# Kernel optimization log

Measured on AMD Instinct MI355X. Metric: run time of the kernel, lower is better.

Reference implementation:

```python
import jax, jax.numpy as jnp
import numpy as np

# WFN symmetry table: symmetry index -> (px, py, pz) angular-momentum exponents
# (s; px,py,pz; 6 cartesian d; 10 cartesian f) as in standard .wfn files.
WFN_SYMMETRY_INDEX = np.array([
    [0, 0, 0],
    [1, 0, 0], [0, 1, 0], [0, 0, 1],
    [2, 0, 0], [0, 2, 0], [0, 0, 2], [1, 1, 0], [1, 0, 1], [0, 1, 1],
    [3, 0, 0], [0, 3, 0], [0, 0, 3], [2, 1, 0], [2, 0, 1], [0, 2, 1],
    [1, 2, 0], [1, 0, 2], [0, 1, 2], [1, 1, 1],
], dtype=np.float32)


def setup_inputs() -> dict:
    key = jax.random.key(0)
    k1, k2, k3, k4, k5 = jax.random.split(key, 5)
    n, ms, na, nps = 16, 4096, 32, 512
    dv = jax.random.normal(k1, (n, ms, na, 3), jnp.float32)          # sample->atom displacement vectors
    centers = jax.random.randint(k2, (n, nps), 0, na)                # primitive -> atom index (-1 = pad)
    exp = jax.random.uniform(k3, (n, nps), jnp.float32)              # GTO exponents (>0)
    sym = jax.random.randint(k4, (n, nps), 0, 20)                    # symmetry index into WFN table
    dm = jax.random.normal(k5, (n, nps, nps), jnp.float32) / nps     # density matrices
    return {"dv": dv, "centers": centers, "exp": exp, "sym": sym, "dm": dm}


def _density(dv, exp, dm, centers, sym):
    # dv: [n,ms,na,3]; exp: [n,np]; dm: [n,np,np]; centers/sym: [n,np] int
    sym_map = jnp.asarray(WFN_SYMMETRY_INDEX)
    valid = centers >= 0                                   # padded primitives marked -1
    c = jnp.where(valid, centers, 0)
    s = jnp.where(valid, sym, 0)
    r2 = jnp.sum(dv * dv, axis=-1)                         # [n,ms,na] squared distances
    r2g = jax.vmap(lambda r, ci: r[:, ci])(r2, c)          # [n,ms,np] gather per primitive
    dvg = jax.vmap(lambda d, ci: d[:, ci])(dv, c)          # [n,ms,np,3]
    pw = sym_map[s]                                        # [n,np,3] angular exponents
    # GTO kernel: dx^px * dy^py * dz^pz * exp(-alpha * r^2)
    ang = jnp.prod(jnp.power(dvg, pw[:, None, :, :]), axis=-1)   # [n,ms,np]
    basis = ang * jnp.exp(-exp[:, None, :] * r2g)
    basis = basis * valid[:, None, :].astype(basis.dtype)        # zero out padded primitives
    # rho = sum_pq basis_p * dm_pq * basis_q (per molecule, per sample point)
    return jnp.einsum('nmp,npq,nmq->nm', basis, dm, basis)


def reference(dv, centers, exp, sym, dm):
    return _density(dv, exp, dm, centers, sym)
```

## Files before the change

kernel.cpp:

```cpp
#include <hip/hip_runtime.h>
#include <stdint.h>

#define NMOL 16
#define MS   4096
#define NA   32
#define NP   512
#define BM   64
#define TBL  65536u

typedef __attribute__((ext_vector_type(4))) float  f32x4;
typedef __attribute__((ext_vector_type(4))) unsigned int u32x4;
typedef __attribute__((ext_vector_type(2))) unsigned int u32x2;
typedef __attribute__((ext_vector_type(8))) short  s16x8;
typedef unsigned int uint;
typedef unsigned short ushort;

#define WS_DMF_OFF   0u
#define WS_DMF_SZ    (16u*512u*512u*2u)
#define WS_M2A_OFF   (WS_DMF_OFF + WS_DMF_SZ)
#define WS_M2A_SZ    (16u*512u*4u)
#define WS_M2B_OFF   (WS_M2A_OFF + WS_M2A_SZ)
#define WS_M2B_SZ    (16u*512u*4u)
#define WS_ALPH_OFF  (WS_M2B_OFF + WS_M2B_SZ)

__device__ __constant__ uint c_pw[20] = {
  0x000,
  0x001, 0x010, 0x100,
  0x002, 0x020, 0x200, 0x011, 0x101, 0x110,
  0x003, 0x030, 0x300, 0x012, 0x102, 0x120, 0x021, 0x201, 0x210, 0x111
};

__device__ __forceinline__ ushort f2bf(float f) {
  uint u = __float_as_uint(f);
  u = u + 0x7fffu + ((u >> 16) & 1u);
  return (ushort)(u >> 16);
}
__device__ __forceinline__ float bflo(uint u) { return __uint_as_float(u << 16); }
__device__ __forceinline__ float bfhi(uint u) { return __uint_as_float(u & 0xFFFF0000u); }
__device__ __forceinline__ float cvt16lo(uint u) {
  float r; asm("v_cvt_f32_f16 %0, %1" : "=v"(r) : "v"(u)); return r;
}
__device__ __forceinline__ float cvt16hi(uint u) {
  uint s = u >> 16; float r; asm("v_cvt_f32_f16 %0, %1" : "=v"(r) : "v"(s)); return r;
}
__device__ __forceinline__ uint pkmul(uint a, uint b) {
  uint r; asm("v_pk_mul_f16 %0, %1, %2" : "=v"(r) : "v"(a), "v"(b)); return r;
}
__device__ __forceinline__ s16x8 mkfrag(u32x2 lo, u32x2 hi) {
  union { uint u[4]; s16x8 v; } x;
  x.u[0] = lo[0]; x.u[1] = lo[1]; x.u[2] = hi[0]; x.u[3] = hi[1];
  return x.v;
}

__global__ void dm_pack(const float* __restrict__ dm, short* __restrict__ dmF) {
  __shared__ float tile[NP * 16];
  const int Q = blockIdx.x, n = blockIdx.y;
  const float* src = dm + (size_t)n * NP * NP + Q * 16;
#pragma unroll
  for (int i = 0; i < 32; ++i) {
    int e = threadIdx.x + 256 * i;
    int p = e >> 4, c = e & 15;
    tile[e] = src[(size_t)p * NP + c];
  }
  __syncthreads();
  short* dst = dmF + ((size_t)(n * 32 + Q) * 16) * 512;
#pragma unroll
  for (int i = 0; i < 4; ++i) {
    int v = threadIdx.x + 256 * i;
    int kblk = v >> 6, l = v & 63;
    int p0 = kblk * 32 + ((l >> 4) << 3);
    int col = l & 15;
    s16x8 o;
#pragma unroll
    for (int j = 0; j < 8; ++j) o[j] = (short)f2bf(tile[(p0 + j) * 16 + col]);
    *(s16x8*)(dst + (size_t)v * 8) = o;
  }
}

__global__ void prep_pack(const int* __restrict__ centers, const int* __restrict__ sym,
                          const float* __restrict__ expg,
                          uint* __restrict__ m2a, uint* __restrict__ m2b,
                          float* __restrict__ alphaS) {
  int i = blockIdx.x * 256 + threadIdx.x;
  int craw = centers[i], s = sym[i];
  bool valid = (craw >= 0);
  uint c = (uint)((valid ? craw : 0) & (NA - 1));
  int si = valid ? s : 0;
  si = (si >= 0 && si < 20) ? si : 0;
  uint pw = c_pw[si];
  uint px = pw & 15u, py = (pw >> 4) & 15u, pz = (pw >> 8) & 15u;
  uint d = px + py + pz;
  uint h[3]; int k = 0;
#pragma unroll
  for (uint ax = 0; ax < 3; ++ax) {
    uint e = (pw >> (4 * ax)) & 15u;
    for (uint r = 0; r < e; ++r) if (k < 3) h[k++] = c * 512u + ax * 128u;
  }
  while (k < 3) h[k++] = c * 512u;
  m2a[i] = h[0] | (h[1] << 16);
  m2b[i] = h[2] | (d << 14) | (c << 16);
  alphaS[i] = (valid ? -expg[i] : -1e5f) * 1.44269504088896f;
}

__launch_bounds__(512, 4)
__global__ void wfn_fused8(const float* __restrict__ dv,
                           const uint* __restrict__ m2aG,
                           const uint* __restrict__ m2bG,
                           const float* __restrict__ alG,
                           const short* __restrict__ dmF,
                           float* __restrict__ out) {
  __shared__ __align__(16) char smem[81920];
  const int t = threadIdx.x;
  const int bid = ((blockIdx.x & 7) << 7) + (blockIdx.x >> 3);
  const int n  = bid >> 6;
  const int m0 = (bid & 63) * BM;

  {
    const float* dvg = dv + (size_t)(n * MS + m0) * (NA * 3);
#pragma unroll
    for (int k = 0; k < 4; ++k) {
      int idx = t + 512 * k;
      int m = idx >> 5, c = idx & 31;
      const float* p = dvg + (m * NA + c) * 3;
      float x = p[0], y = p[1], z = p[2];
      float r2 = fmaf(x, x, fmaf(y, y, z * z));
      uint base = TBL + (uint)c * 512u
                + ((uint)((m >> 3) ^ (c & 7)) << 4) + (uint)((m & 7) << 1);
      *(_Float16*)(smem + base)       = (_Float16)x;
      *(_Float16*)(smem + base + 128) = (_Float16)y;
      *(_Float16*)(smem + base + 256) = (_Float16)z;
      *(_Float16*)(smem + base + 384) = (_Float16)r2;
    }
  }
  __syncthreads();

  {
    const int p = t;
    const uint ma = m2aG[n * NP + p], mb = m2bG[n * NP + p];
    const float al = alG[n * NP + p];
    const uint h0 = ma & 0xFFFFu, h1 = ma >> 16;
    const uint h2 = mb & 0x3FFFu;
    const uint d  = (mb >> 14) & 3u;
    const uint cs = (h0 >> 9) & 7u;
    const uint rh = (h0 & 0xFE00u) + 384u;
    const bool ge2 = (d >= 2), eq3 = (d == 3), eq0 = (d == 0);
    const uint wbase = ((uint)(p >> 5) << 10) + (((uint)(p >> 2) & 1u) << 9)
                     + ((((uint)p & 31u) >> 3) << 7) + (((uint)p & 3u) << 5);
#pragma unroll
    for (int j = 0; j < 8; ++j) {
      uint off = (uint)((j ^ (int)cs) << 4);
      u32x4 q0 = *(const u32x4*)(smem + TBL + h0 + off);
      u32x4 q1 = *(const u32x4*)(smem + TBL + h1 + off);
      u32x4 q2 = *(const u32x4*)(smem + TBL + h2 + off);
      u32x4 qr = *(const u32x4*)(smem + TBL + rh + off);
      uint res[4];
#pragma unroll
      for (int w = 0; w < 4; ++w) {
        uint m_ = q0[w];
        uint t1 = pkmul(m_, q1[w]);  m_ = ge2 ? t1 : m_;
        uint t2 = pkmul(m_, q2[w]);  m_ = eq3 ? t2 : m_;
        m_ = eq0 ? 0x3C003C00u : m_;
        float r2l = cvt16lo(qr[w]), r2h = cvt16hi(qr[w]);
        float a0 = al * r2l, a1 = al * r2h;
        float e0, e1;
        asm("v_exp_f32 %0, %1" : "=v"(e0) : "v"(a0));
        asm("v_exp_f32 %0, %1" : "=v"(e1) : "v"(a1));
        float v0 = cvt16lo(m_) * e0, v1 = cvt16hi(m_) * e1;
        asm("v_cvt_pk_bf16_f32 %0, %1, %2" : "=v"(res[w]) : "v"(v0), "v"(v1));
      }
      *(u32x4*)(smem + wbase + ((uint)(j >> 1) << 14) + ((uint)(j & 1) << 4))
          = *(u32x4*)res;
    }
  }
  __syncthreads();

  const int lane = t & 63, wv = t >> 6, li = lane & 15, kg = lane >> 4;
  const uint lane8 = (uint)lane << 3;
  const short* dmFn = dmF + (size_t)n * (32 * 16 * 512);

  f32x4 acc[4][4];
#pragma unroll
  for (int rf = 0; rf < 4; ++rf)
#pragma unroll
    for (int qf = 0; qf < 4; ++qf)
      acc[rf][qf] = (f32x4){0.f, 0.f, 0.f, 0.f};

  const short* bptr[4];
#pragma unroll
  for (int qf = 0; qf < 4; ++qf)
    bptr[qf] = dmFn + ((size_t)((wv * 4 + qf) * 16) * 512) + lane * 8;

#pragma unroll 2
  for (int kblk = 0; kblk < 16; ++kblk) {
    s16x8 bf[4];
#pragma unroll
    for (int qf = 0; qf < 4; ++qf)
      bf[qf] = *(const s16x8*)(bptr[qf] + kblk * 512);
    uint ak = lane8 + ((uint)kblk << 10);
    u32x2 l0, g0, l1, g1, l2, g2, l3, g3;
    asm volatile("ds_read_b64_tr_b16 %0, %1 offset:0"     : "=v"(l0) : "v"(ak));
    asm volatile("ds_read_b64_tr_b16 %0, %1 offset:512"   : "=v"(g0) : "v"(ak));
    asm volatile("ds_read_b64_tr_b16 %0, %1 offset:16384" : "=v"(l1) : "v"(ak));
    asm volatile("ds_read_b64_tr_b16 %0, %1 offset:16896" : "=v"(g1) : "v"(ak));
    asm volatile("ds_read_b64_tr_b16 %0, %1 offset:32768" : "=v"(l2) : "v"(ak));
    asm volatile("ds_read_b64_tr_b16 %0, %1 offset:33280" : "=v"(g2) : "v"(ak));
    asm volatile("ds_read_b64_tr_b16 %0, %1 offset:49152" : "=v"(l3) : "v"(ak));
    asm volatile("ds_read_b64_tr_b16 %0, %1 offset:49664" : "=v"(g3) : "v"(ak));
    asm volatile("s_waitcnt lgkmcnt(0)");
    __builtin_amdgcn_sched_barrier(0);
    s16x8 af[4];
    af[0] = mkfrag(l0, g0); af[1] = mkfrag(l1, g1);
    af[2] = mkfrag(l2, g2); af[3] = mkfrag(l3, g3);
#pragma unroll
    for (int rf = 0; rf < 4; ++rf)
#pragma unroll
      for (int qf = 0; qf < 4; ++qf)
        acc[rf][qf] = __builtin_amdgcn_mfma_f32_16x16x32_bf16(
            af[rf], bf[qf], acc[rf][qf], 0, 0, 0);
  }

  float part[16];
#pragma unroll
  for (int x = 0; x < 16; ++x) part[x] = 0.0f;
  uint qp[4];
#pragma unroll
  for (int qf = 0; qf < 4; ++qf) {
    int q = wv * 64 + qf * 16 + li;
    qp[qf] = ((uint)(q >> 5) << 10) + (((uint)(q >> 2) & 1u) << 9)
           + (((uint)(q & 31) >> 3) << 7) + ((uint)(q & 3) << 5) + ((uint)kg << 3);
  }
#pragma unroll
  for (int rf = 0; rf < 4; ++rf) {
#pragma unroll
    for (int qf = 0; qf < 4; ++qf) {
      u32x2 dq = *(const u32x2*)(smem + ((uint)rf << 14) + qp[qf]);
      part[rf * 4 + 0] = fmaf(acc[rf][qf][0], bflo(dq[0]), part[rf * 4 + 0]);
      part[rf * 4 + 1] = fmaf(acc[rf][qf][1], bfhi(dq[0]), part[rf * 4 + 1]);
      part[rf * 4 + 2] = fmaf(acc[rf][qf][2], bflo(dq[1]), part[rf * 4 + 2]);
      part[rf * 4 + 3] = fmaf(acc[rf][qf][3], bfhi(dq[1]), part[rf * 4 + 3]);
    }
  }

  __syncthreads();
#pragma unroll
  for (int x = 0; x < 16; ++x) {
    float v = part[x];
    v += __shfl_xor(v, 1);
    v += __shfl_xor(v, 2);
    v += __shfl_xor(v, 4);
    v += __shfl_xor(v, 8);
    part[x] = v;
  }
  float* rbuf = (float*)smem;
  if (li == 0) {
#pragma unroll
    for (int rf = 0; rf < 4; ++rf)
#pragma unroll
      for (int jj = 0; jj < 4; ++jj)
        rbuf[wv * 64 + rf * 16 + kg * 4 + jj] = part[rf * 4 + jj];
  }
  __syncthreads();
  if (t < BM) {
    float s = 0.0f;
#pragma unroll
    for (int w = 0; w < 8; ++w) s += rbuf[w * 64 + t];
    out[(size_t)n * MS + m0 + t] = s;
  }
}

extern "C" void kernel_launch(void* const* d_in, const int* in_sizes, int n_in,
                              void* d_out, int out_size, void* d_ws, size_t ws_size,
                              hipStream_t stream) {
  const float* dv      = (const float*)d_in[0];
  const int*   centers = (const int*)d_in[1];
  const float* expg    = (const float*)d_in[2];
  const int*   sym     = (const int*)d_in[3];
  const float* dm      = (const float*)d_in[4];
  float* out = (float*)d_out;

  char* ws = (char*)d_ws;
  short* dmF    = (short*)(ws + WS_DMF_OFF);
  uint*  m2a    = (uint*)(ws + WS_M2A_OFF);
  uint*  m2b    = (uint*)(ws + WS_M2B_OFF);
  float* alphaS = (float*)(ws + WS_ALPH_OFF);

  dm_pack<<<dim3(32, NMOL), 256, 0, stream>>>(dm, dmF);
  prep_pack<<<dim3(32), 256, 0, stream>>>(centers, sym, expg, m2a, m2b, alphaS);
  wfn_fused8<<<dim3(NMOL * (MS / BM)), 512, 0, stream>>>(dv, m2a, m2b, alphaS, dmF, out);
}
```

Before: 56.89 us.

## Exploit density-matrix symmetry via triangular folding and merge prep into dm_pack

The density matrix is folded into an upper-triangular form (dm + dm^T off the diagonal, zero below it), so the quadratic form needs only about half the MFMA k-blocks. The q-fragment assignment per wave is interleaved so the triangular work is spread evenly across waves. The prep_pack work moves into dm_pack to save a kernel launch, and the basis build skips LDS reads for zero-degree primitives. The price is a second transposed dm tile load in dm_pack, more per-iteration branching in the MFMA loop, and a bit of extra bf16 rounding on the summed off-diagonal terms.

After: 51.92 us. 8.7% less time.

```diff
diff --git a/kernel.cpp b/kernel.cpp
--- a/kernel.cpp
+++ b/kernel.cpp
@@ -52,54 +52,69 @@
   return x.v;
 }
 
-__global__ void dm_pack(const float* __restrict__ dm, short* __restrict__ dmF) {
+__global__ void dm_pack(const float* __restrict__ dm, short* __restrict__ dmF,
+                        const int* __restrict__ centers, const int* __restrict__ sym,
+                        const float* __restrict__ expg,
+                        uint* __restrict__ m2a, uint* __restrict__ m2b,
+                        float* __restrict__ alphaS) {
   __shared__ float tile[NP * 16];
+  __shared__ float tileT[16 * (NP + 2)];
   const int Q = blockIdx.x, n = blockIdx.y;
-  const float* src = dm + (size_t)n * NP * NP + Q * 16;
+  const int t = threadIdx.x;
+  const float* base = dm + (size_t)n * NP * NP;
+  const float* src  = base + Q * 16;
 #pragma unroll
   for (int i = 0; i < 32; ++i) {
-    int e = threadIdx.x + 256 * i;
+    int e = t + 256 * i;
     int p = e >> 4, c = e & 15;
     tile[e] = src[(size_t)p * NP + c];
   }
+  const float* srcT = base + (size_t)(Q * 16) * NP;
+#pragma unroll
+  for (int i = 0; i < 32; ++i) {
+    int e = t + 256 * i;
+    tileT[(e >> 9) * (NP + 2) + (e & 511)] = srcT[e];
+  }
+  if (n == 0) {
+    int i = Q * 256 + t;
+    int craw = centers[i], s = sym[i];
+    bool valid = (craw >= 0);
+    uint c = (uint)((valid ? craw : 0) & (NA - 1));
+    int si = valid ? s : 0;
+    si = (si >= 0 && si < 20) ? si : 0;
+    uint pw = c_pw[si];
+    uint d = (pw & 15u) + ((pw >> 4) & 15u) + ((pw >> 8) & 15u);
+    uint h[3]; int k = 0;
+#pragma unroll
+    for (uint ax = 0; ax < 3; ++ax) {
+      uint e = (pw >> (4 * ax)) & 15u;
+      for (uint r = 0; r < e; ++r) if (k < 3) h[k++] = c * 512u + ax * 128u;
+    }
+    while (k < 3) h[k++] = c * 512u;
+    m2a[i] = h[0] | (h[1] << 16);
+    m2b[i] = h[2] | (d << 14) | (c << 16);
+    alphaS[i] = (valid ? -expg[i] : -1e5f) * 1.44269504088896f;
+  }
   __syncthreads();
   short* dst = dmF + ((size_t)(n * 32 + Q) * 16) * 512;
 #pragma unroll
   for (int i = 0; i < 4; ++i) {
-    int v = threadIdx.x + 256 * i;
+    int v = t + 256 * i;
     int kblk = v >> 6, l = v & 63;
     int p0 = kblk * 32 + ((l >> 4) << 3);
     int col = l & 15;
+    int q = Q * 16 + col;
     s16x8 o;
 #pragma unroll
-    for (int j = 0; j < 8; ++j) o[j] = (short)f2bf(tile[(p0 + j) * 16 + col]);
+    for (int j = 0; j < 8; ++j) {
+      int p = p0 + j;
+      float w = 0.0f;
+      if (p < q)       w = tile[p * 16 + col] + tileT[col * (NP + 2) + p];
+      else if (p == q) w = tile[p * 16 + col];
+      o[j] = (short)f2bf(w);
+    }
     *(s16x8*)(dst + (size_t)v * 8) = o;
   }
-}
-
-__global__ void prep_pack(const int* __restrict__ centers, const int* __restrict__ sym,
-                          const float* __restrict__ expg,
-                          uint* __restrict__ m2a, uint* __restrict__ m2b,
-                          float* __restrict__ alphaS) {
-  int i = blockIdx.x * 256 + threadIdx.x;
-  int craw = centers[i], s = sym[i];
-  bool valid = (craw >= 0);
-  uint c = (uint)((valid ? craw : 0) & (NA - 1));
-  int si = valid ? s : 0;
-  si = (si >= 0 && si < 20) ? si : 0;
-  uint pw = c_pw[si];
-  uint px = pw & 15u, py = (pw >> 4) & 15u, pz = (pw >> 8) & 15u;
-  uint d = px + py + pz;
-  uint h[3]; int k = 0;
-#pragma unroll
-  for (uint ax = 0; ax < 3; ++ax) {
-    uint e = (pw >> (4 * ax)) & 15u;
-    for (uint r = 0; r < e; ++r) if (k < 3) h[k++] = c * 512u + ax * 128u;
-  }
-  while (k < 3) h[k++] = c * 512u;
-  m2a[i] = h[0] | (h[1] << 16);
-  m2b[i] = h[2] | (d << 14) | (c << 16);
-  alphaS[i] = (valid ? -expg[i] : -1e5f) * 1.44269504088896f;
 }
 
 __launch_bounds__(512, 4)
@@ -149,17 +164,17 @@
 #pragma unroll
     for (int j = 0; j < 8; ++j) {
       uint off = (uint)((j ^ (int)cs) << 4);
-      u32x4 q0 = *(const u32x4*)(smem + TBL + h0 + off);
-      u32x4 q1 = *(const u32x4*)(smem + TBL + h1 + off);
-      u32x4 q2 = *(const u32x4*)(smem + TBL + h2 + off);
       u32x4 qr = *(const u32x4*)(smem + TBL + rh + off);
+      u32x4 q0, q1, q2;
+      if (!eq0) q0 = *(const u32x4*)(smem + TBL + h0 + off);
+      if (ge2)  q1 = *(const u32x4*)(smem + TBL + h1 + off);
+      if (eq3)  q2 = *(const u32x4*)(smem + TBL + h2 + off);
       uint res[4];
 #pragma unroll
       for (int w = 0; w < 4; ++w) {
-        uint m_ = q0[w];
-        uint t1 = pkmul(m_, q1[w]);  m_ = ge2 ? t1 : m_;
-        uint t2 = pkmul(m_, q2[w]);  m_ = eq3 ? t2 : m_;
-        m_ = eq0 ? 0x3C003C00u : m_;
+        uint m_ = eq0 ? 0x3C003C00u : q0[w];
+        if (ge2) m_ = pkmul(m_, q1[w]);
+        if (eq3) m_ = pkmul(m_, q2[w]);
         float r2l = cvt16lo(qr[w]), r2h = cvt16hi(qr[w]);
         float a0 = al * r2l, a1 = al * r2h;
         float e0, e1;
@@ -185,17 +200,14 @@
     for (int qf = 0; qf < 4; ++qf)
       acc[rf][qf] = (f32x4){0.f, 0.f, 0.f, 0.f};
 
-  const short* bptr[4];
-#pragma unroll
-  for (int qf = 0; qf < 4; ++qf)
-    bptr[qf] = dmFn + ((size_t)((wv * 4 + qf) * 16) * 512) + lane * 8;
-
-#pragma unroll 2
-  for (int kblk = 0; kblk < 16; ++kblk) {
-    s16x8 bf[4];
-#pragma unroll
-    for (int qf = 0; qf < 4; ++qf)
-      bf[qf] = *(const s16x8*)(bptr[qf] + kblk * 512);
+  const short* bp0 = dmFn + ((size_t)((wv)      * 16) * 512) + lane * 8;
+  const short* bp1 = dmFn + ((size_t)((wv + 8)  * 16) * 512) + lane * 8;
+  const short* bp2 = dmFn + ((size_t)((wv + 16) * 16) * 512) + lane * 8;
+  const short* bp3 = dmFn + ((size_t)((wv + 24) * 16) * 512) + lane * 8;
+  const int kq0 = wv >> 1, kq1 = (wv + 8) >> 1, kq2 = (wv + 16) >> 1;
+  const int kmaxw = (wv + 24) >> 1;
+
+  for (int kblk = 0; kblk <= kmaxw; ++kblk) {
     uint ak = lane8 + ((uint)kblk << 10);
     u32x2 l0, g0, l1, g1, l2, g2, l3, g3;
     asm volatile("ds_read_b64_tr_b16 %0, %1 offset:0"     : "=v"(l0) : "v"(ak));
@@ -206,17 +218,36 @@
     asm volatile("ds_read_b64_tr_b16 %0, %1 offset:33280" : "=v"(g2) : "v"(ak));
     asm volatile("ds_read_b64_tr_b16 %0, %1 offset:49152" : "=v"(l3) : "v"(ak));
     asm volatile("ds_read_b64_tr_b16 %0, %1 offset:49664" : "=v"(g3) : "v"(ak));
+    s16x8 bf0, bf1, bf2, bf3;
+    if (kblk <= kq0) bf0 = *(const s16x8*)(bp0 + kblk * 512);
+    if (kblk <= kq1) bf1 = *(const s16x8*)(bp1 + kblk * 512);
+    if (kblk <= kq2) bf2 = *(const s16x8*)(bp2 + kblk * 512);
+    bf3 = *(const s16x8*)(bp3 + kblk * 512);
     asm volatile("s_waitcnt lgkmcnt(0)");
     __builtin_amdgcn_sched_barrier(0);
     s16x8 af[4];
     af[0] = mkfrag(l0, g0); af[1] = mkfrag(l1, g1);
     af[2] = mkfrag(l2, g2); af[3] = mkfrag(l3, g3);
+    __builtin_amdgcn_s_setprio(1);
+    if (kblk <= kq0) {
+#pragma unroll
+      for (int rf = 0; rf < 4; ++rf)
+        acc[rf][0] = __builtin_amdgcn_mfma_f32_16x16x32_bf16(af[rf], bf0, acc[rf][0], 0, 0, 0);
+    }
+    if (kblk <= kq1) {
+#pragma unroll
+      for (int rf = 0; rf < 4; ++rf)
+        acc[rf][1] = __builtin_amdgcn_mfma_f32_16x16x32_bf16(af[rf], bf1, acc[rf][1], 0, 0, 0);
+    }
+    if (kblk <= kq2) {
+#pragma unroll
+      for (int rf = 0; rf < 4; ++rf)
+        acc[rf][2] = __builtin_amdgcn_mfma_f32_16x16x32_bf16(af[rf], bf2, acc[rf][2], 0, 0, 0);
+    }
 #pragma unroll
     for (int rf = 0; rf < 4; ++rf)
-#pragma unroll
-      for (int qf = 0; qf < 4; ++qf)
-        acc[rf][qf] = __builtin_amdgcn_mfma_f32_16x16x32_bf16(
-            af[rf], bf[qf], acc[rf][qf], 0, 0, 0);
+      acc[rf][3] = __builtin_amdgcn_mfma_f32_16x16x32_bf16(af[rf], bf3, acc[rf][3], 0, 0, 0);
+    __builtin_amdgcn_s_setprio(0);
   }
 
   float part[16];
@@ -225,7 +256,7 @@
   uint qp[4];
 #pragma unroll
   for (int qf = 0; qf < 4; ++qf) {
-    int q = wv * 64 + qf * 16 + li;
+    int q = (wv + 8 * qf) * 16 + li;
     qp[qf] = ((uint)(q >> 5) << 10) + (((uint)(q >> 2) & 1u) << 9)
            + (((uint)(q & 31) >> 3) << 7) + ((uint)(q & 3) << 5) + ((uint)kg << 3);
   }
@@ -284,7 +315,7 @@
   uint*  m2b    = (uint*)(ws + WS_M2B_OFF);
   float* alphaS = (float*)(ws + WS_ALPH_OFF);
 
-  dm_pack<<<dim3(32, NMOL), 256, 0, stream>>>(dm, dmF);
-  prep_pack<<<dim3(32), 256, 0, stream>>>(centers, sym, expg, m2a, m2b, alphaS);
+  dm_pack<<<dim3(32, NMOL), 256, 0, stream>>>(dm, dmF, centers, sym, expg,
+                                              m2a, m2b, alphaS);
   wfn_fused8<<<dim3(NMOL * (MS / BM)), 512, 0, stream>>>(dv, m2a, m2b, alphaS, dmF, out);
 }
```
